# Performance work log

Hardware: AMD Instinct MI355X
Metric: run time of the kernel (lower is better)

The kernel has to match this reference:

```python
import jax, jax.numpy as jnp
import numpy as np

N_HEADS = 16


def setup_inputs() -> dict:
    key = jax.random.key(0)
    k1, k2, k3, k4 = jax.random.split(key, 4)
    B, W, c, C = 4, 1024, 32, 1024
    x = jax.random.normal(k1, (B, W, c, C), dtype=jnp.float32)
    w_pos_emb = jax.random.normal(k2, (W, C), dtype=jnp.float32)
    attn_w = jax.random.normal(k3, (3 * C, C), dtype=jnp.float32) * (1.0 / np.sqrt(C))
    proj_w = jax.random.normal(k4, (C, C), dtype=jnp.float32) * (1.0 / np.sqrt(C))
    attention_mask = jnp.ones((B, W, c), dtype=jnp.int32)
    return {"x": x, "w_pos_emb": w_pos_emb, "attn_w": attn_w,
            "proj_w": proj_w, "attention_mask": attention_mask}


def reference(x, w_pos_emb, attn_w, proj_w, attention_mask):
    B, W, c, C = x.shape
    H = N_HEADS
    Dh = C // H
    # last-token pooling: one-hot of (count-1) over char axis, multiply-sum
    last_ix = attention_mask.sum(-1) - 1                      # [B, W]
    oh = jax.nn.one_hot(last_ix, c, dtype=x.dtype)            # [B, W, c]
    word = jnp.einsum('bwcd,bwc->bwd', x, oh)                 # [B, W, C]
    word = word + w_pos_emb                                   # first_time pos-emb add
    # QKV projection (torch Linear: y = x @ W^T)
    qkv = jnp.einsum('bwd,ed->bwe', word, attn_w)             # [B, W, 3C]
    q, k, v = jnp.split(qkv, 3, axis=-1)
    def heads(t):
        return t.reshape(B, W, H, Dh).transpose(0, 2, 1, 3)   # [B, H, W, Dh]
    q, k, v = heads(q), heads(k), heads(v)
    scale = 1.0 / np.sqrt(Dh).astype(np.float32)
    scores = jnp.einsum('bhqd,bhkd->bhqk', q, k) * scale      # [B, H, W, W]
    causal = jnp.tril(jnp.ones((W, W), dtype=bool))
    scores = jnp.where(causal, scores, jnp.finfo(scores.dtype).min)
    probs = jax.nn.softmax(scores, axis=-1)
    out = jnp.einsum('bhqk,bhkd->bhqd', probs, v)             # [B, H, W, Dh]
    out = out.transpose(0, 2, 1, 3).reshape(B, W, C)
    out = jnp.einsum('bwd,ed->bwe', out, proj_w)              # c_proj
    # dropout is identity in eval mode
    return (word, out)
```

## Files before the change

kernel.cpp:

```cpp
#include <hip/hip_runtime.h>

#define BB 4
#define WW 1024
#define CDIM 1024
#define CCH 32
#define NH 16
#define DH 64
#define MROWS (BB * WW)

typedef __bf16 bf16x8 __attribute__((ext_vector_type(8)));
typedef float f32x4 __attribute__((ext_vector_type(4)));

static __device__ __forceinline__ unsigned short f2bf(float f) {
    union { float f; unsigned u; } v; v.f = f;
    unsigned r = v.u + 0x7fffu + ((v.u >> 16) & 1u);
    return (unsigned short)(r >> 16);
}

#if defined(__has_builtin)
#if __has_builtin(__builtin_amdgcn_global_load_lds)
#define HAVE_GLL 1
#endif
#endif

#ifdef HAVE_GLL
static __device__ __forceinline__ void gload16(const void* g, void* l) {
    __builtin_amdgcn_global_load_lds(
        (const __attribute__((address_space(1))) unsigned int*)g,
        (__attribute__((address_space(3))) unsigned int*)l, 16, 0, 0);
}
#endif

__global__ __launch_bounds__(256) void prep_kernel(const float* __restrict__ aw,
                                                   const float* __restrict__ pw,
                                                   const float* __restrict__ x,
                                                   const float* __restrict__ pos,
                                                   const int* __restrict__ mask,
                                                   unsigned short* __restrict__ awb,
                                                   unsigned short* __restrict__ pwb,
                                                   float* __restrict__ word_f32,
                                                   unsigned short* __restrict__ word_bf) {
    int blk = blockIdx.x;
    if (blk < 4096) {
        int g = blk * 256 + threadIdx.x;
        const int NA4 = 3 * CDIM * CDIM / 4;
        if (g < NA4) {
            float4 vv = ((const float4*)aw)[g];
            ushort4 o = { f2bf(vv.x), f2bf(vv.y), f2bf(vv.z), f2bf(vv.w) };
            ((ushort4*)awb)[g] = o;
        } else {
            int kk = g - NA4;
            float4 vv = ((const float4*)pw)[kk];
            ushort4 o = { f2bf(vv.x), f2bf(vv.y), f2bf(vv.z), f2bf(vv.w) };
            ((ushort4*)pwb)[kk] = o;
        }
    } else {
        int bw = blk - 4096;
        int w = bw & (WW - 1);
        __shared__ int s_last;
        if (threadIdx.x == 0) {
            int ssum = 0;
            for (int j = 0; j < CCH; ++j) ssum += mask[bw * CCH + j];
            s_last = ssum - 1;
        }
        __syncthreads();
        int last = s_last;
        const float4* xr = (const float4*)(x + ((size_t)bw * CCH + (last < 0 ? 0 : last)) * CDIM);
        const float4* pr = (const float4*)(pos + (size_t)w * CDIM);
        int d4 = threadIdx.x;
        float4 xv = (last >= 0) ? xr[d4] : float4{0.f, 0.f, 0.f, 0.f};
        float4 pv = pr[d4];
        float4 vv = { xv.x + pv.x, xv.y + pv.y, xv.z + pv.z, xv.w + pv.w };
        ((float4*)(word_f32 + (size_t)bw * CDIM))[d4] = vv;
        ushort4 o = { f2bf(vv.x), f2bf(vv.y), f2bf(vv.z), f2bf(vv.w) };
        ((ushort4*)(word_bf + (size_t)bw * CDIM))[d4] = o;
    }
}

template <int EPI, int BM, int BN, int WRN, int WCN, int MI, int NI>
__global__ __launch_bounds__(256) void gemm_nt_kernel(const unsigned short* __restrict__ A,
                                                      const unsigned short* __restrict__ Bt,
                                                      int Mdim, int Ndim, int Kdim,
                                                      unsigned short* __restrict__ qb,
                                                      unsigned short* __restrict__ kb,
                                                      unsigned short* __restrict__ vb,
                                                      float* __restrict__ outp) {
    __shared__ unsigned short As[BM * 64];
    __shared__ unsigned short Bs[BN * 64];
    int t = threadIdx.x;
    int wid = t >> 6, lane = t & 63;
    int wr = wid / WCN, wc = wid % WCN;
    int mbase = blockIdx.y * BM, nbase = blockIdx.x * BN;
    int lr = lane & 15, lg = lane >> 4;
    f32x4 acc[MI][NI] = {};

#ifdef HAVE_GLL
    int csrc = ((lane & 7) ^ (lane >> 3)) * 8;
    int rofs = lane >> 3;
    const int TOT = (BM + BN) / 8;
#endif

    for (int kt = 0; kt < Kdim; kt += 64) {
        __syncthreads();
#ifdef HAVE_GLL
        for (int cch = wid; cch < TOT; cch += 4) {
            if (cch < BM / 8)
                gload16(A + (size_t)(mbase + cch * 8 + rofs) * Kdim + kt + csrc, &As[cch * 8 * 64]);
            else {
                int cb = cch - BM / 8;
                gload16(Bt + (size_t)(nbase + cb * 8 + rofs) * Kdim + kt + csrc, &Bs[cb * 8 * 64]);
            }
        }
#else
        for (int s = 0; s < (BM + BN) / 32; ++s) {
            int f = s * 256 + t;
            int row = f >> 3, c8 = (f & 7) * 8;
            if (row < BM)
                *(int4*)&As[row * 64 + (c8 ^ ((row & 7) << 3))] =
                    *(const int4*)&A[(size_t)(mbase + row) * Kdim + kt + c8];
            else {
                int rb = row - BM;
                *(int4*)&Bs[rb * 64 + (c8 ^ ((rb & 7) << 3))] =
                    *(const int4*)&Bt[(size_t)(nbase + rb) * Kdim + kt + c8];
            }
        }
#endif
        __syncthreads();
        for (int ks = 0; ks < 2; ++ks) {
            bf16x8 af[MI], bfr[NI];
            int cc = ks * 32 + lg * 8;
            for (int mi = 0; mi < MI; ++mi) {
                int r = wr * (MI * 16) + mi * 16 + lr;
                af[mi] = *(const bf16x8*)&As[r * 64 + (cc ^ ((r & 7) << 3))];
            }
            for (int ni = 0; ni < NI; ++ni) {
                int r = wc * (NI * 16) + ni * 16 + lr;
                bfr[ni] = *(const bf16x8*)&Bs[r * 64 + (cc ^ ((r & 7) << 3))];
            }
            __builtin_amdgcn_s_setprio(1);
            for (int mi = 0; mi < MI; ++mi)
                for (int ni = 0; ni < NI; ++ni)
                    acc[mi][ni] = __builtin_amdgcn_mfma_f32_16x16x32_bf16(af[mi], bfr[ni], acc[mi][ni], 0, 0, 0);
            __builtin_amdgcn_s_setprio(0);
        }
    }
    for (int mi = 0; mi < MI; ++mi)
        for (int ni = 0; ni < NI; ++ni)
            for (int i = 0; i < 4; ++i) {
                int row = mbase + wr * (MI * 16) + mi * 16 + lg * 4 + i;
                int col = nbase + wc * (NI * 16) + ni * 16 + lr;
                float v = acc[mi][ni][i];
                if (EPI == 0) {
                    int sect = col >> 10, ch = col & 1023, hh = ch >> 6, dd = ch & 63;
                    int bI = row >> 10, wI = row & 1023;
                    size_t dst = ((size_t)(bI * NH + hh) * WW + wI) * DH + dd;
                    if (sect == 0) qb[dst] = f2bf(v * 0.125f);
                    else if (sect == 1) kb[dst] = f2bf(v);
                    else vb[dst] = f2bf(v);
                } else {
                    outp[(size_t)row * Ndim + col] = v;
                }
            }
}

__global__ __launch_bounds__(512) void attn_kernel(const unsigned short* __restrict__ q,
                                                   const unsigned short* __restrict__ k,
                                                   const unsigned short* __restrict__ v,
                                                   unsigned short* __restrict__ aout) {
    __shared__ unsigned short Ks[64 * 64];
    __shared__ unsigned short Vt[64 * 64];
    __shared__ unsigned short Ps0[128 * 64];
    __shared__ unsigned short Ps1[128 * 64];
    int t = threadIdx.x;
    int wid = t >> 6, lane = t & 63;
    int lr = lane & 15, lg = lane >> 4;
    int bh = blockIdx.y, bI = bh >> 4, hI = bh & 15;
    int p = blockIdx.x;
    int qa = p * 128, qbv = (7 - p) * 128;
    int nktA = 2 * p + 2, nktB = 16 - 2 * p;
    const float EXP2C = 1.44269504f;
    const float SHIFTC = 28.8539008f;

    bf16x8 qfA[2], qfB[2];
    {
        const unsigned short* qg = q + (size_t)bh * WW * DH;
        int r = wid * 16 + lr;
        for (int ks = 0; ks < 2; ++ks) {
            qfA[ks] = *(const bf16x8*)&qg[(size_t)(qa + r) * DH + ks * 32 + lg * 8];
            qfB[ks] = *(const bf16x8*)&qg[(size_t)(qbv + r) * DH + ks * 32 + lg * 8];
        }
    }

    float rlA[4] = {0.f, 0.f, 0.f, 0.f}, rlB[4] = {0.f, 0.f, 0.f, 0.f};
    f32x4 oA[4] = {}, oB[4] = {};

    const unsigned short* kbase = k + (size_t)bh * WW * DH;
    const unsigned short* vbase = v + (size_t)bh * WW * DH;
    int dp = (t & 31) * 2, kb8 = (t >> 5) & 7;
    int tt = t & 255;
    int krow = tt >> 3, kc8 = (tt & 7) * 8;

    unsigned int vr[8]; int4 kr0, kr1;
    auto prefetch = [&](int tn) {
        if (wid < 4) {
            const unsigned short* vg = vbase + (size_t)tn * 64 * DH;
#pragma unroll
            for (int j = 0; j < 8; ++j)
                vr[j] = *(const unsigned int*)&vg[(size_t)(kb8 * 8 + j) * DH + dp];
        } else {
            const unsigned short* kg = kbase + (size_t)tn * 64 * DH;
            kr0 = *(const int4*)&kg[(size_t)krow * DH + kc8];
            kr1 = *(const int4*)&kg[(size_t)(krow + 32) * DH + kc8];
        }
    };
    prefetch(0);

    auto process = [&](const bf16x8* qf, int qbase, float* rl, unsigned short* PsX, int tki) {
        f32x4 s[4] = {};
        for (int ks = 0; ks < 2; ++ks) {
            bf16x8 bfr[4];
            int cc = ks * 32 + lg * 8;
            for (int ni = 0; ni < 4; ++ni) {
                int r = ni * 16 + lr;
                bfr[ni] = *(const bf16x8*)&Ks[r * 64 + (cc ^ ((r & 7) << 3))];
            }
            __builtin_amdgcn_s_setprio(1);
            for (int ni = 0; ni < 4; ++ni)
                s[ni] = __builtin_amdgcn_mfma_f32_16x16x32_bf16(qf[ks], bfr[ni], s[ni], 0, 0, 0);
            __builtin_amdgcn_s_setprio(0);
        }
        int rowbase = qbase + wid * 16 + lg * 4;
        if (tki * 64 + 63 > qbase + wid * 16) {
            for (int ni = 0; ni < 4; ++ni)
                for (int i = 0; i < 4; ++i) {
                    int ki = tki * 64 + ni * 16 + lr;
                    if (ki > rowbase + i) s[ni][i] = -1e30f;
                }
        }
#pragma unroll
        for (int ni = 0; ni < 4; ++ni)
#pragma unroll
            for (int i = 0; i < 4; ++i) {
                float pe = __builtin_amdgcn_exp2f(fmaf(s[ni][i], EXP2C, -SHIFTC));
                s[ni][i] = pe;
                rl[i] += pe;
            }
        for (int ni = 0; ni < 4; ++ni)
            for (int i = 0; i < 4; ++i) {
                int r = wid * 16 + lg * 4 + i;
                PsX[r * 64 + ((ni * 16 + lr) ^ ((r & 7) << 3))] = f2bf(s[ni][i]);
            }
    };

    auto pvacc = [&](f32x4* o, const unsigned short* PsX) {
        for (int ks = 0; ks < 2; ++ks) {
            int cc = ks * 32 + lg * 8;
            int r = wid * 16 + lr;
            bf16x8 pa = *(const bf16x8*)&PsX[r * 64 + (cc ^ ((r & 7) << 3))];
            bf16x8 vbf[4];
            for (int di = 0; di < 4; ++di) {
                int rv = di * 16 + lr;
                vbf[di] = *(const bf16x8*)&Vt[rv * 64 + (cc ^ ((rv & 7) << 3))];
            }
            __builtin_amdgcn_s_setprio(1);
            for (int di = 0; di < 4; ++di)
                o[di] = __builtin_amdgcn_mfma_f32_16x16x32_bf16(pa, vbf[di], o[di], 0, 0, 0);
            __builtin_amdgcn_s_setprio(0);
        }
    };

    for (int tki = 0; tki < nktB; ++tki) {
        __syncthreads();
        if (wid < 4) {
            unsigned short lo[8], hi[8];
#pragma unroll
            for (int j = 0; j < 8; ++j) { lo[j] = (unsigned short)(vr[j] & 0xffffu);
                                          hi[j] = (unsigned short)(vr[j] >> 16); }
            *(int4*)&Vt[dp * 64 + ((kb8 * 8) ^ ((dp & 7) << 3))] = *(int4*)lo;
            int d1 = dp + 1;
            *(int4*)&Vt[d1 * 64 + ((kb8 * 8) ^ ((d1 & 7) << 3))] = *(int4*)hi;
        } else {
            *(int4*)&Ks[krow * 64 + (kc8 ^ ((krow & 7) << 3))] = kr0;
            int r1 = krow + 32;
            *(int4*)&Ks[r1 * 64 + (kc8 ^ ((r1 & 7) << 3))] = kr1;
        }
        if (tki + 1 < nktB) prefetch(tki + 1);
        __syncthreads();

        bool wB = (tki * 64 <= qbv + wid * 16 + 15);
        bool wA = (tki < nktA) && (tki * 64 <= qa + wid * 16 + 15);
        if (wB) process(qfB, qbv, rlB, Ps1, tki);
        if (wA) process(qfA, qa, rlA, Ps0, tki);
        if (wB) pvacc(oB, Ps1);
        if (wA) pvacc(oA, Ps0);
    }

#pragma unroll
    for (int i = 0; i < 4; ++i) {
        for (int d = 8; d >= 1; d >>= 1) rlA[i] += __shfl_xor(rlA[i], d);
        for (int d = 8; d >= 1; d >>= 1) rlB[i] += __shfl_xor(rlB[i], d);
    }
    for (int di = 0; di < 4; ++di)
        for (int i = 0; i < 4; ++i) {
            int dd = di * 16 + lr;
            int qrA = qa + wid * 16 + lg * 4 + i;
            int qrB = qbv + wid * 16 + lg * 4 + i;
            aout[((size_t)bI * WW + qrA) * CDIM + hI * DH + dd] = f2bf(oA[di][i] / rlA[i]);
            aout[((size_t)bI * WW + qrB) * CDIM + hI * DH + dd] = f2bf(oB[di][i] / rlB[i]);
        }
}

extern "C" void kernel_launch(void* const* d_in, const int* in_sizes, int n_in,
                              void* d_out, int out_size, void* d_ws, size_t ws_size,
                              hipStream_t stream) {
    const float* x    = (const float*)d_in[0];
    const float* pos  = (const float*)d_in[1];
    const float* aw   = (const float*)d_in[2];
    const float* pw   = (const float*)d_in[3];
    const int*   mask = (const int*)d_in[4];
    float* out = (float*)d_out;
    float* word_f32 = out;
    float* proj_out = out + (size_t)MROWS * CDIM;

    const size_t MB = 1u << 20;
    char* ws = (char*)d_ws;
    unsigned short* word_bf = (unsigned short*)(ws);
    unsigned short* awb     = (unsigned short*)(ws + 8 * MB);
    unsigned short* pwb     = (unsigned short*)(ws + 14 * MB);
    unsigned short* qb      = (unsigned short*)(ws + 16 * MB);
    unsigned short* kb      = (unsigned short*)(ws + 24 * MB);
    unsigned short* vb      = (unsigned short*)(ws + 32 * MB);
    unsigned short* aob     = (unsigned short*)(ws + 40 * MB);

    prep_kernel<<<8192, 256, 0, stream>>>(aw, pw, x, pos, mask, awb, pwb, word_f32, word_bf);
    gemm_nt_kernel<0, 128, 128, 2, 2, 4, 4><<<dim3(3 * CDIM / 128, MROWS / 128), 256, 0, stream>>>(
        word_bf, awb, MROWS, 3 * CDIM, CDIM, qb, kb, vb, nullptr);
    attn_kernel<<<dim3(4, BB * NH), 512, 0, stream>>>(qb, kb, vb, aob);
    gemm_nt_kernel<1, 128, 64, 4, 1, 2, 4><<<dim3(CDIM / 64, MROWS / 128), 256, 0, stream>>>(
        aob, pwb, MROWS, CDIM, CDIM, nullptr, nullptr, nullptr, proj_out);
}
```

Baseline: 97.16 us.

## Remap block IDs per XCD for L2 locality and hoist attention LDS fragment loads

Both GEMMs and the attention kernel now use a 1D grid and remap the block ID so that blocks landing on the same XCD (bid & 7) share N-columns or heads. This aims to improve L2 reuse of B tiles and K/V data. The attention loop also loads the K and V fragments from LDS once per tile, not once per query group (A/B), which removes duplicate LDS reads at the cost of more live registers.

```diff
diff --git a/kernel.cpp b/kernel.cpp
--- a/kernel.cpp
+++ b/kernel.cpp
@@ -77,7 +77,7 @@
     }
 }
 
-template <int EPI, int BM, int BN, int WRN, int WCN, int MI, int NI>
+template <int EPI, int BM, int BN, int WRN, int WCN, int MI, int NI, int NBX, int CW>
 __global__ __launch_bounds__(256) void gemm_nt_kernel(const unsigned short* __restrict__ A,
                                                       const unsigned short* __restrict__ Bt,
                                                       int Mdim, int Ndim, int Kdim,
@@ -90,7 +90,11 @@
     int t = threadIdx.x;
     int wid = t >> 6, lane = t & 63;
     int wr = wid / WCN, wc = wid % WCN;
-    int mbase = blockIdx.y * BM, nbase = blockIdx.x * BN;
+    int bid = blockIdx.x;
+    int xcd = bid & 7, idx = bid >> 3;
+    int bx = xcd * CW + idx % CW;
+    int by = idx / CW;
+    int mbase = by * BM, nbase = bx * BN;
     int lr = lane & 15, lg = lane >> 4;
     f32x4 acc[MI][NI] = {};
 
@@ -174,8 +178,11 @@
     int t = threadIdx.x;
     int wid = t >> 6, lane = t & 63;
     int lr = lane & 15, lg = lane >> 4;
-    int bh = blockIdx.y, bI = bh >> 4, hI = bh & 15;
-    int p = blockIdx.x;
+    int bid = blockIdx.x;
+    int xcd = bid & 7, idx = bid >> 3;
+    int bh = xcd + ((idx >> 2) << 3);
+    int p = idx & 3;
+    int bI = bh >> 4, hI = bh & 15;
     int qa = p * 128, qbv = (7 - p) * 128;
     int nktA = 2 * p + 2, nktB = 16 - 2 * p;
     const float EXP2C = 1.44269504f;
@@ -215,20 +222,16 @@
     };
     prefetch(0);
 
-    auto process = [&](const bf16x8* qf, int qbase, float* rl, unsigned short* PsX, int tki) {
+    auto process = [&](const bf16x8* qf, const bf16x8 (*bfr)[4], int qbase,
+                       float* rl, unsigned short* PsX, int tki) {
         f32x4 s[4] = {};
-        for (int ks = 0; ks < 2; ++ks) {
-            bf16x8 bfr[4];
-            int cc = ks * 32 + lg * 8;
-            for (int ni = 0; ni < 4; ++ni) {
-                int r = ni * 16 + lr;
-                bfr[ni] = *(const bf16x8*)&Ks[r * 64 + (cc ^ ((r & 7) << 3))];
-            }
-            __builtin_amdgcn_s_setprio(1);
+        __builtin_amdgcn_s_setprio(1);
+#pragma unroll
+        for (int ks = 0; ks < 2; ++ks)
+#pragma unroll
             for (int ni = 0; ni < 4; ++ni)
-                s[ni] = __builtin_amdgcn_mfma_f32_16x16x32_bf16(qf[ks], bfr[ni], s[ni], 0, 0, 0);
-            __builtin_amdgcn_s_setprio(0);
-        }
+                s[ni] = __builtin_amdgcn_mfma_f32_16x16x32_bf16(qf[ks], bfr[ks][ni], s[ni], 0, 0, 0);
+        __builtin_amdgcn_s_setprio(0);
         int rowbase = qbase + wid * 16 + lg * 4;
         if (tki * 64 + 63 > qbase + wid * 16) {
             for (int ni = 0; ni < 4; ++ni)
@@ -252,19 +255,16 @@
             }
     };
 
-    auto pvacc = [&](f32x4* o, const unsigned short* PsX) {
+    auto pvacc = [&](f32x4* o, const unsigned short* PsX, const bf16x8 (*vbf)[4]) {
+#pragma unroll
         for (int ks = 0; ks < 2; ++ks) {
             int cc = ks * 32 + lg * 8;
             int r = wid * 16 + lr;
             bf16x8 pa = *(const bf16x8*)&PsX[r * 64 + (cc ^ ((r & 7) << 3))];
-            bf16x8 vbf[4];
-            for (int di = 0; di < 4; ++di) {
-                int rv = di * 16 + lr;
-                vbf[di] = *(const bf16x8*)&Vt[rv * 64 + (cc ^ ((rv & 7) << 3))];
-            }
             __builtin_amdgcn_s_setprio(1);
+#pragma unroll
             for (int di = 0; di < 4; ++di)
-                o[di] = __builtin_amdgcn_mfma_f32_16x16x32_bf16(pa, vbf[di], o[di], 0, 0, 0);
+                o[di] = __builtin_amdgcn_mfma_f32_16x16x32_bf16(pa, vbf[ks][di], o[di], 0, 0, 0);
             __builtin_amdgcn_s_setprio(0);
         }
     };
@@ -289,10 +289,32 @@
 
         bool wB = (tki * 64 <= qbv + wid * 16 + 15);
         bool wA = (tki < nktA) && (tki * 64 <= qa + wid * 16 + 15);
-        if (wB) process(qfB, qbv, rlB, Ps1, tki);
-        if (wA) process(qfA, qa, rlA, Ps0, tki);
-        if (wB) pvacc(oB, Ps1);
-        if (wA) pvacc(oA, Ps0);
+
+        bf16x8 bfr[2][4];
+#pragma unroll
+        for (int ks = 0; ks < 2; ++ks) {
+            int cc = ks * 32 + lg * 8;
+#pragma unroll
+            for (int ni = 0; ni < 4; ++ni) {
+                int r = ni * 16 + lr;
+                bfr[ks][ni] = *(const bf16x8*)&Ks[r * 64 + (cc ^ ((r & 7) << 3))];
+            }
+        }
+        if (wB) process(qfB, bfr, qbv, rlB, Ps1, tki);
+        if (wA) process(qfA, bfr, qa, rlA, Ps0, tki);
+
+        bf16x8 vbf[2][4];
+#pragma unroll
+        for (int ks = 0; ks < 2; ++ks) {
+            int cc = ks * 32 + lg * 8;
+#pragma unroll
+            for (int di = 0; di < 4; ++di) {
+                int rv = di * 16 + lr;
+                vbf[ks][di] = *(const bf16x8*)&Vt[rv * 64 + (cc ^ ((rv & 7) << 3))];
+            }
+        }
+        if (wB) pvacc(oB, Ps1, vbf);
+        if (wA) pvacc(oA, Ps0, vbf);
     }
 
 #pragma unroll
@@ -333,9 +355,9 @@
     unsigned short* aob     = (unsigned short*)(ws + 40 * MB);
 
     prep_kernel<<<8192, 256, 0, stream>>>(aw, pw, x, pos, mask, awb, pwb, word_f32, word_bf);
-    gemm_nt_kernel<0, 128, 128, 2, 2, 4, 4><<<dim3(3 * CDIM / 128, MROWS / 128), 256, 0, stream>>>(
+    gemm_nt_kernel<0, 128, 128, 2, 2, 4, 4, 24, 3><<<768, 256, 0, stream>>>(
         word_bf, awb, MROWS, 3 * CDIM, CDIM, qb, kb, vb, nullptr);
-    attn_kernel<<<dim3(4, BB * NH), 512, 0, stream>>>(qb, kb, vb, aob);
-    gemm_nt_kernel<1, 128, 64, 4, 1, 2, 4><<<dim3(CDIM / 64, MROWS / 128), 256, 0, stream>>>(
+    attn_kernel<<<256, 512, 0, stream>>>(qb, kb, vb, aob);
+    gemm_nt_kernel<1, 128, 64, 4, 1, 2, 4, 16, 2><<<512, 256, 0, stream>>>(
         aob, pwb, MROWS, CDIM, CDIM, nullptr, nullptr, nullptr, proj_out);
 }
```

After: 95.73 us. No clear change (-1.5%).
